# Kernel optimization log

Measured on AMD Instinct MI355X. Metric: run time of the kernel, lower is better.

## Reference

```python
import jax, jax.numpy as jnp
import numpy as np

B, N, NFG, NFR = 512, 64, 1024, 256
OH, OW = 87, 157
POS_THRESHOLD = 0.2


def setup_inputs() -> dict:
    key = jax.random.key(0)
    ks = jax.random.split(key, 7)
    feats = jax.random.normal(ks[0], (B, N, NFG), dtype=jnp.float32)
    # boxes (x1,y1,x2,y2) in image coordinates
    boxes = jax.random.uniform(ks[1], (B, N, 4), dtype=jnp.float32)
    scale = jnp.array([OW, OH, OW, OH], dtype=jnp.float32)
    boxes = boxes * scale
    s_in = 1.0 / np.sqrt(NFG)
    W_theta = jax.random.normal(ks[2], (NFG, NFR), dtype=jnp.float32) * s_in
    b_theta = jnp.zeros((NFR,), dtype=jnp.float32)
    W_phi = jax.random.normal(ks[3], (NFG, NFR), dtype=jnp.float32) * s_in
    b_phi = jnp.zeros((NFR,), dtype=jnp.float32)
    W_gcn = jax.random.normal(ks[4], (NFG, NFG), dtype=jnp.float32) * s_in
    return {
        "graph_boxes_features": feats,
        "boxes_in_flat": boxes,
        "W_theta": W_theta,
        "b_theta": b_theta,
        "W_phi": W_phi,
        "b_phi": b_phi,
        "W_gcn": W_gcn,
    }


def reference(graph_boxes_features, boxes_in_flat, W_theta, b_theta, W_phi, b_phi, W_gcn):
    nfr = W_theta.shape[-1]
    # box centers [B,N,2]
    cx = (boxes_in_flat[..., 0] + boxes_in_flat[..., 2]) * 0.5
    cy = (boxes_in_flat[..., 1] + boxes_in_flat[..., 3]) * 0.5
    pos = jnp.stack([cx, cy], axis=-1)  # [B,N,2]
    # pairwise euclidean distances [B,N,N]
    diff = pos[:, :, None, :] - pos[:, None, :, :]
    dist = jnp.sqrt(jnp.sum(diff * diff, axis=-1))
    position_mask = dist > (POS_THRESHOLD * OW)

    theta = jnp.einsum('bnf,fr->bnr', graph_boxes_features, W_theta) + b_theta
    phi = jnp.einsum('bnf,fr->bnr', graph_boxes_features, W_phi) + b_phi
    sim = jnp.einsum('bnr,bmr->bnm', theta, phi) / jnp.sqrt(jnp.asarray(nfr, theta.dtype))
    logits = jnp.where(position_mask, -jnp.inf, sim)
    relation_graph = jax.nn.softmax(logits, axis=2)  # [B,N,N]

    agg = jnp.einsum('bnm,bmf->bnf', relation_graph, graph_boxes_features)
    out = jax.nn.relu(jnp.einsum('bnf,fg->bng', agg, W_gcn))
    return out, relation_graph
```

## Files before the change

### kernel.cpp

```cpp
#include <hip/hip_runtime.h>
#include <hip/hip_bf16.h>
#include <math.h>

#define BB   512
#define NN   64
#define NFG  1024
#define NFR  256
#define MM   (BB * NN)
#define RG_OFF 33554432L

typedef __attribute__((ext_vector_type(8))) short bf16x8;
typedef __attribute__((ext_vector_type(4))) float f32x4;
typedef __attribute__((ext_vector_type(8))) unsigned short u16x8;

__device__ inline unsigned short f2bf(float f) {
    union { float f; unsigned u; } v; v.f = f;
    unsigned u = v.u;
    return (unsigned short)((u + 0x7FFFu + ((u >> 16) & 1u)) >> 16);
}

__device__ inline void gld_lds16(const unsigned short* g, unsigned short* l) {
    __builtin_amdgcn_global_load_lds((const __attribute__((address_space(1))) void*)g,
                                     (__attribute__((address_space(3))) void*)l, 16, 0, 0);
}


__device__ void tcast_body(const float* __restrict__ in, unsigned short* __restrict__ out,
                           int K, int N, int bx, int by, float tile[32][33]) {
    const int t  = threadIdx.x;
    const int tx = t & 31, ty = t >> 5;
    const int k0 = by * 32, n0 = bx * 32;
#pragma unroll
    for (int r = 0; r < 4; ++r)
        tile[ty + r * 8][tx] = in[(long)(k0 + ty + r * 8) * N + n0 + tx];
    __syncthreads();
#pragma unroll
    for (int r = 0; r < 4; ++r)
        out[(long)(n0 + ty + r * 8) * K + k0 + tx] = f2bf(tile[tx][ty + r * 8]);
}

__global__ __launch_bounds__(256)
void prep(const float* __restrict__ feats, unsigned short* __restrict__ featsb,
          const float* __restrict__ W_theta, const float* __restrict__ W_phi,
          const float* __restrict__ W_gcn,
          unsigned short* __restrict__ Wtp, unsigned short* __restrict__ Wgt,
          const float* __restrict__ bt, const float* __restrict__ bp,
          float* __restrict__ bias512) {
    __shared__ float tile[32][33];
    const int bid = blockIdx.x;
    const int t   = threadIdx.x;
    if (bid < 16384) {
        long i = ((long)bid * 256 + t) * 8;
        if (i + 8 <= 33554432L) {
            f32x4 a = *(const f32x4*)(feats + i);
            f32x4 b = *(const f32x4*)(feats + i + 4);
            u16x8 o;
#pragma unroll
            for (int c = 0; c < 4; ++c) { o[c] = f2bf(a[c]); o[4 + c] = f2bf(b[c]); }
            *(u16x8*)(featsb + i) = o;
        }
    } else if (bid < 16640) {
        int r = bid - 16384;
        tcast_body(W_theta, Wtp, 1024, 256, r & 7, r >> 3, tile);
    } else if (bid < 16896) {
        int r = bid - 16640;
        tcast_body(W_phi, Wtp + 256 * 1024, 1024, 256, r & 7, r >> 3, tile);
    } else if (bid < 17920) {
        int r = bid - 16896;
        tcast_body(W_gcn, Wgt, 1024, 1024, r & 31, r >> 5, tile);
    } else {
        bias512[t]       = bt[t];
        bias512[t + 256] = bp[t];
    }
}


template<int RELU, int STORE_BF16, int SWIZ, int LOG_FAST>
__global__ __launch_bounds__(256, 4)
void gemm_bt(const unsigned short* __restrict__ A, const unsigned short* __restrict__ Bt,
             const float* __restrict__ bias, void* __restrict__ Cout,
             int M, int N, int K) {
    __shared__ __align__(16) unsigned short As[128 * 64];
    __shared__ __align__(16) unsigned short Bs[128 * 64];
    const int t    = threadIdx.x;
    const int lane = t & 63;
    const int w    = t >> 6;
    const int l15  = lane & 15;
    const int q    = lane >> 4;

    long mtile, ntile;
    if (SWIZ == 1) {
        long linear = (long)blockIdx.y * gridDim.x + blockIdx.x;
        int  xcd  = (int)(linear & 7);
        long slot = linear >> 3;
        mtile = slot & ((1 << LOG_FAST) - 1);
        ntile = (long)xcd * (gridDim.y >> 3) + (slot >> LOG_FAST);
    } else if (SWIZ == 2) {
        long linear = (long)blockIdx.y * gridDim.x + blockIdx.x;
        int  xcd  = (int)(linear & 7);
        long slot = linear >> 3;
        ntile = slot & ((1 << LOG_FAST) - 1);
        mtile = (long)xcd * (gridDim.x >> 3) + (slot >> LOG_FAST);
    } else {
        mtile = blockIdx.x; ntile = blockIdx.y;
    }
    const long tileM = mtile * 128;
    const long tileN = ntile * 128;
    const int wm = (w & 1) * 64;
    const int wn = (w >> 1) * 64;

    f32x4 acc[4][4] = {};

    const int rS = t >> 3;
    const int cS = (t & 7) ^ (rS & 7);
    const unsigned short* gA = A  + (tileM + rS) * (long)K + cS * 8;
    const unsigned short* gB = Bt + (tileN + rS) * (long)K + cS * 8;

    for (int kt = 0; kt < K; kt += 64) {
        __syncthreads();
#pragma unroll
        for (int i = 0; i < 4; ++i) {
            gld_lds16(gA + (long)i * 32 * K + kt, As + (i * 256 + w * 64) * 8);
            gld_lds16(gB + (long)i * 32 * K + kt, Bs + (i * 256 + w * 64) * 8);
        }
        __syncthreads();
#pragma unroll
        for (int ks = 0; ks < 2; ++ks) {
            const int slot = (ks * 4 + q) ^ (l15 & 7);
            bf16x8 af[4], bf[4];
#pragma unroll
            for (int mi = 0; mi < 4; ++mi)
                af[mi] = *(const bf16x8*)(As + (wm + mi * 16 + l15) * 64 + slot * 8);
#pragma unroll
            for (int ni = 0; ni < 4; ++ni)
                bf[ni] = *(const bf16x8*)(Bs + (wn + ni * 16 + l15) * 64 + slot * 8);
#pragma unroll
            for (int mi = 0; mi < 4; ++mi)
#pragma unroll
                for (int ni = 0; ni < 4; ++ni)
                    acc[mi][ni] = __builtin_amdgcn_mfma_f32_16x16x32_bf16(af[mi], bf[ni],
                                                                          acc[mi][ni], 0, 0, 0);
        }
    }

#pragma unroll
    for (int mi = 0; mi < 4; ++mi) {
#pragma unroll
        for (int ni = 0; ni < 4; ++ni) {
            long row0 = tileM + wm + mi * 16 + q * 4;
            long col  = tileN + wn + ni * 16 + l15;
            float bv = bias ? bias[col] : 0.f;
#pragma unroll
            for (int r = 0; r < 4; ++r) {
                float v = acc[mi][ni][r] + bv;
                if (RELU) v = fmaxf(v, 0.f);
                long idx = (row0 + r) * N + col;
                if (STORE_BF16) ((unsigned short*)Cout)[idx] = f2bf(v);
                else            ((float*)Cout)[idx] = v;
            }
        }
    }
}


__global__ __launch_bounds__(256)
void fused_softmax_out(const unsigned short* __restrict__ thetaphi,
                       const float* __restrict__ boxes,
                       const unsigned short* __restrict__ HtT,
                       float* __restrict__ rg_out,
                       float* __restrict__ out) {
    __shared__ __align__(16) float sim_s[64][68];
    __shared__ __align__(16) unsigned short Pb[64][72];
    __shared__ float cxs[64], cys[64];
    const int t    = threadIdx.x;
    const int b    = blockIdx.x >> 1;
    const int gh   = blockIdx.x & 1;
    const int lane = t & 63;
    const int w    = t >> 6;
    const int l15  = lane & 15;
    const int q    = lane >> 4;

    const unsigned short* HtB = HtT + (long)b * 64;
    bf16x8 hb0[8], hb1[8];
#pragma unroll
    for (int nt = 0; nt < 8; ++nt) {
        const int g0 = gh * 512 + w * 128 + nt * 16;
        const unsigned short* hp = HtB + (long)(g0 + l15) * 32768 + q * 8;
        hb0[nt] = *(const bf16x8*)(hp);
        hb1[nt] = *(const bf16x8*)(hp + 32);
    }
    __builtin_amdgcn_sched_barrier(0);

    if (t < 64) {
        float4 bx = *(const float4*)(boxes + ((long)b * 64 + t) * 4);
        cxs[t] = (bx.x + bx.z) * 0.5f;
        cys[t] = (bx.y + bx.w) * 0.5f;
    }

    {
        f32x4 acc[4] = {};
        const unsigned short* thA = thetaphi + ((long)b * 64 + w * 16 + l15) * 512 + q * 8;
        const unsigned short* thB = thetaphi + ((long)b * 64 + l15) * 512 + 256 + q * 8;
#pragma unroll
        for (int kt = 0; kt < 256; kt += 32) {
            bf16x8 a = *(const bf16x8*)(thA + kt);
#pragma unroll
            for (int ni = 0; ni < 4; ++ni) {
                bf16x8 bb = *(const bf16x8*)(thB + (long)ni * 16 * 512 + kt);
                acc[ni] = __builtin_amdgcn_mfma_f32_16x16x32_bf16(a, bb, acc[ni], 0, 0, 0);
            }
        }
#pragma unroll
        for (int ni = 0; ni < 4; ++ni)
#pragma unroll
            for (int r = 0; r < 4; ++r)
                sim_s[w * 16 + q * 4 + r][ni * 16 + l15] = acc[ni][r] * 0.0625f;
    }
    __syncthreads();

    {
        const int i  = t >> 2;
        const int j0 = (t & 3) * 16;
        const float cxi = cxs[i], cyi = cys[i];
        const float thr = (float)(0.2 * 157.0);
        float vals[16];
        float mx = -__builtin_inff();
#pragma unroll
        for (int jj = 0; jj < 16; ++jj) {
            int j = j0 + jj;
            float dx = cxi - cxs[j];
            float dy = cyi - cys[j];
            bool msk = sqrtf(dx * dx + dy * dy) > thr;
            float s = msk ? -__builtin_inff() : sim_s[i][j];
            vals[jj] = s;
            mx = fmaxf(mx, s);
        }
        mx = fmaxf(mx, __shfl_xor(mx, 1, 64));
        mx = fmaxf(mx, __shfl_xor(mx, 2, 64));
        float sum = 0.f;
#pragma unroll
        for (int jj = 0; jj < 16; ++jj) {
            float e = (vals[jj] == -__builtin_inff()) ? 0.f : __expf(vals[jj] - mx);
            vals[jj] = e;
            sum += e;
        }
        sum += __shfl_xor(sum, 1, 64);
        sum += __shfl_xor(sum, 2, 64);
        float inv = 1.f / sum;
#pragma unroll
        for (int jj = 0; jj < 16; ++jj) {
            int j = j0 + jj;
            float p = vals[jj] * inv;
            if (gh == 0) rg_out[((long)b * 64 + i) * 64 + j] = p;
            Pb[i][j] = f2bf(p);
        }
    }
    __syncthreads();

    {
        float* outB = out + (long)b * 65536;
        bf16x8 af[4][2];
#pragma unroll
        for (int mi = 0; mi < 4; ++mi)
#pragma unroll
            for (int kk = 0; kk < 2; ++kk)
                af[mi][kk] = *(const bf16x8*)(&Pb[mi * 16 + l15][kk * 32 + q * 8]);
#pragma unroll
        for (int nt = 0; nt < 8; ++nt) {
            const int g0 = gh * 512 + w * 128 + nt * 16;
#pragma unroll
            for (int mi = 0; mi < 4; ++mi) {
                f32x4 acc = {};
                acc = __builtin_amdgcn_mfma_f32_16x16x32_bf16(af[mi][0], hb0[nt], acc, 0, 0, 0);
                acc = __builtin_amdgcn_mfma_f32_16x16x32_bf16(af[mi][1], hb1[nt], acc, 0, 0, 0);
#pragma unroll
                for (int r = 0; r < 4; ++r)
                    outB[(long)(mi * 16 + q * 4 + r) * 1024 + g0 + l15] = fmaxf(acc[r], 0.f);
            }
        }
    }
}


extern "C" void kernel_launch(void* const* d_in, const int* in_sizes, int n_in,
                              void* d_out, int out_size, void* d_ws, size_t ws_size,
                              hipStream_t stream) {
    const float* feats   = (const float*)d_in[0];
    const float* boxes   = (const float*)d_in[1];
    const float* W_theta = (const float*)d_in[2];
    const float* b_theta = (const float*)d_in[3];
    const float* W_phi   = (const float*)d_in[4];
    const float* b_phi   = (const float*)d_in[5];
    const float* W_gcn   = (const float*)d_in[6];
    float* out = (float*)d_out;

    char* ws = (char*)d_ws;
    unsigned short* featsb   = (unsigned short*)(ws);
    unsigned short* thetaphi = (unsigned short*)(ws + 67108864);
    unsigned short* HtT      = (unsigned short*)(ws + 100663296);
    unsigned short* Wtp      = (unsigned short*)(ws + 167772160);
    unsigned short* Wgt      = (unsigned short*)(ws + 168820736);
    float*          bias512  = (float*)(ws + 170917888);

    prep<<<17921, 256, 0, stream>>>(feats, featsb, W_theta, W_phi, W_gcn,
                                    Wtp, Wgt, b_theta, b_phi, bias512);

    gemm_bt<0, 1, 2, 2><<<dim3(256, 4), 256, 0, stream>>>(featsb, Wtp, bias512, thetaphi,
                                                          MM, 512, 1024);
    gemm_bt<0, 1, 1, 3><<<dim3(8, 256), 256, 0, stream>>>(Wgt, featsb, nullptr, HtT,
                                                          1024, MM, 1024);
    fused_softmax_out<<<BB * 2, 256, 0, stream>>>(thetaphi, boxes, HtT, out + RG_OFF, out);
}
```

Baseline: 417.9 us.

## Make softmax-output kernel wave-local with rolling HtT prefetch and no block barriers

Repartitions the final fused kernel so each wave owns 16 output rows across all 512 columns of its half. Softmax and P@H data then stay inside one wave, so both __syncthreads become wave-level fences, and box centers move from shared memory to lane shuffles. The B-operand registers shrink to a 6-deep ring that is refilled while MFMAs run, which allows 4 blocks per CU via launch bounds. relation_graph stores are vectorized to 16 bytes. In exchange, every wave now reads the whole HtT slice, four times the previous global/L2 traffic for that operand.

```diff
diff --git a/kernel.cpp b/kernel.cpp
--- a/kernel.cpp
+++ b/kernel.cpp
@@ -22,6 +22,12 @@
 __device__ inline void gld_lds16(const unsigned short* g, unsigned short* l) {
     __builtin_amdgcn_global_load_lds((const __attribute__((address_space(1))) void*)g,
                                      (__attribute__((address_space(3))) void*)l, 16, 0, 0);
+}
+
+__device__ inline void wave_fence() {
+    asm volatile("" ::: "memory");
+    __builtin_amdgcn_wave_barrier();
+    __builtin_amdgcn_sched_barrier(0);
 }
 
 
@@ -163,7 +169,7 @@
 }
 
 
-__global__ __launch_bounds__(256)
+__global__ __launch_bounds__(256, 4)
 void fused_softmax_out(const unsigned short* __restrict__ thetaphi,
                        const float* __restrict__ boxes,
                        const unsigned short* __restrict__ HtT,
@@ -171,7 +177,6 @@
                        float* __restrict__ out) {
     __shared__ __align__(16) float sim_s[64][68];
     __shared__ __align__(16) unsigned short Pb[64][72];
-    __shared__ float cxs[64], cys[64];
     const int t    = threadIdx.x;
     const int b    = blockIdx.x >> 1;
     const int gh   = blockIdx.x & 1;
@@ -181,20 +186,21 @@
     const int q    = lane >> 4;
 
     const unsigned short* HtB = HtT + (long)b * 64;
-    bf16x8 hb0[8], hb1[8];
-#pragma unroll
-    for (int nt = 0; nt < 8; ++nt) {
-        const int g0 = gh * 512 + w * 128 + nt * 16;
+    bf16x8 hb0[6], hb1[6];
+#pragma unroll
+    for (int nt = 0; nt < 6; ++nt) {
+        const int g0 = gh * 512 + nt * 16;
         const unsigned short* hp = HtB + (long)(g0 + l15) * 32768 + q * 8;
         hb0[nt] = *(const bf16x8*)(hp);
         hb1[nt] = *(const bf16x8*)(hp + 32);
     }
     __builtin_amdgcn_sched_barrier(0);
 
-    if (t < 64) {
-        float4 bx = *(const float4*)(boxes + ((long)b * 64 + t) * 4);
-        cxs[t] = (bx.x + bx.z) * 0.5f;
-        cys[t] = (bx.y + bx.w) * 0.5f;
+    float cx, cy;
+    {
+        float4 bx = *(const float4*)(boxes + ((long)b * 64 + lane) * 4);
+        cx = (bx.x + bx.z) * 0.5f;
+        cy = (bx.y + bx.w) * 0.5f;
     }
 
     {
@@ -216,20 +222,21 @@
             for (int r = 0; r < 4; ++r)
                 sim_s[w * 16 + q * 4 + r][ni * 16 + l15] = acc[ni][r] * 0.0625f;
     }
-    __syncthreads();
+    wave_fence();
 
     {
         const int i  = t >> 2;
         const int j0 = (t & 3) * 16;
-        const float cxi = cxs[i], cyi = cys[i];
+        const float cxi = __shfl(cx, i & 63, 64);
+        const float cyi = __shfl(cy, i & 63, 64);
         const float thr = (float)(0.2 * 157.0);
         float vals[16];
         float mx = -__builtin_inff();
 #pragma unroll
         for (int jj = 0; jj < 16; ++jj) {
             int j = j0 + jj;
-            float dx = cxi - cxs[j];
-            float dy = cyi - cys[j];
+            float dx = cxi - __shfl(cx, j, 64);
+            float dy = cyi - __shfl(cy, j, 64);
             bool msk = sqrtf(dx * dx + dy * dy) > thr;
             float s = msk ? -__builtin_inff() : sim_s[i][j];
             vals[jj] = s;
@@ -247,36 +254,40 @@
         sum += __shfl_xor(sum, 1, 64);
         sum += __shfl_xor(sum, 2, 64);
         float inv = 1.f / sum;
+        f32x4 pv[4];
 #pragma unroll
         for (int jj = 0; jj < 16; ++jj) {
-            int j = j0 + jj;
             float p = vals[jj] * inv;
-            if (gh == 0) rg_out[((long)b * 64 + i) * 64 + j] = p;
-            Pb[i][j] = f2bf(p);
-        }
-    }
-    __syncthreads();
+            pv[jj >> 2][jj & 3] = p;
+            Pb[i][j0 + jj] = f2bf(p);
+        }
+        if (gh == 0) {
+            float* rgR = rg_out + ((long)b * 64 + i) * 64 + j0;
+#pragma unroll
+            for (int c = 0; c < 4; ++c) *(f32x4*)(rgR + c * 4) = pv[c];
+        }
+    }
+    wave_fence();
 
     {
-        float* outB = out + (long)b * 65536;
-        bf16x8 af[4][2];
-#pragma unroll
-        for (int mi = 0; mi < 4; ++mi)
-#pragma unroll
-            for (int kk = 0; kk < 2; ++kk)
-                af[mi][kk] = *(const bf16x8*)(&Pb[mi * 16 + l15][kk * 32 + q * 8]);
-#pragma unroll
-        for (int nt = 0; nt < 8; ++nt) {
-            const int g0 = gh * 512 + w * 128 + nt * 16;
-#pragma unroll
-            for (int mi = 0; mi < 4; ++mi) {
-                f32x4 acc = {};
-                acc = __builtin_amdgcn_mfma_f32_16x16x32_bf16(af[mi][0], hb0[nt], acc, 0, 0, 0);
-                acc = __builtin_amdgcn_mfma_f32_16x16x32_bf16(af[mi][1], hb1[nt], acc, 0, 0, 0);
-#pragma unroll
-                for (int r = 0; r < 4; ++r)
-                    outB[(long)(mi * 16 + q * 4 + r) * 1024 + g0 + l15] = fmaxf(acc[r], 0.f);
+        bf16x8 af0 = *(const bf16x8*)(&Pb[w * 16 + l15][q * 8]);
+        bf16x8 af1 = *(const bf16x8*)(&Pb[w * 16 + l15][32 + q * 8]);
+        float* outR = out + (long)b * 65536 + (long)(w * 16 + q * 4) * 1024 + gh * 512 + l15;
+#pragma unroll
+        for (int nt = 0; nt < 32; ++nt) {
+            const int s = nt % 6;
+            f32x4 acc = {};
+            acc = __builtin_amdgcn_mfma_f32_16x16x32_bf16(af0, hb0[s], acc, 0, 0, 0);
+            acc = __builtin_amdgcn_mfma_f32_16x16x32_bf16(af1, hb1[s], acc, 0, 0, 0);
+            if (nt + 6 < 32) {
+                const int g0 = gh * 512 + (nt + 6) * 16;
+                const unsigned short* hp = HtB + (long)(g0 + l15) * 32768 + q * 8;
+                hb0[s] = *(const bf16x8*)(hp);
+                hb1[s] = *(const bf16x8*)(hp + 32);
             }
+#pragma unroll
+            for (int r = 0; r < 4; ++r)
+                outR[(long)r * 1024 + nt * 16] = fmaxf(acc[r], 0.f);
         }
     }
 }
```

New measurement: 416.3 us. No clear change (-0.4%).
